# Optimization experiments

Hardware: AMD Instinct MI355X
Metric: run time of the kernel (lower is better)

The kernel has to match this reference:

```python
import jax, jax.numpy as jnp
import numpy as np

HIDDEN = 512
NHEADS = 8
ALPHA = 0.1
NUM_HOP = 4
MASK_VAL = -16384.0
LN_EPS = 1e-5


def setup_inputs() -> dict:
    key = jax.random.key(0)
    ks = jax.random.split(key, 10)
    B, N, H = 8, 1024, HIDDEN
    s = 1.0 / np.sqrt(H)
    x = jax.random.normal(ks[0], (B, N, H), dtype=jnp.float32)
    adj = jax.random.randint(ks[1], (B, N, N), 0, 2, dtype=jnp.int32)
    Wq = jax.random.uniform(ks[2], (H, H), jnp.float32, -s, s)
    bq = jax.random.uniform(ks[3], (H,), jnp.float32, -s, s)
    Wk = jax.random.uniform(ks[4], (H, H), jnp.float32, -s, s)
    bk = jax.random.uniform(ks[5], (H,), jnp.float32, -s, s)
    Wv = jax.random.uniform(ks[6], (H, H), jnp.float32, -s, s)
    bv = jax.random.uniform(ks[7], (H,), jnp.float32, -s, s)
    gamma = jnp.ones((H,), jnp.float32)
    beta = jnp.zeros((H,), jnp.float32)
    return {"x": x, "adj": adj, "Wq": Wq, "bq": bq, "Wk": Wk, "bk": bk,
            "Wv": Wv, "bv": bv, "gamma": gamma, "beta": beta}


def reference(x, adj, Wq, bq, Wk, bk, Wv, bv, gamma, beta):
    B, N, H = x.shape
    u = H // NHEADS
    # torch Linear: y = x @ W^T + b
    q = x @ Wq.T + bq  # [B,N,H]
    k = x @ Wk.T + bk
    v = x @ Wv.T + bv
    # split hidden into contiguous head chunks (matches per-head slicing)
    qh = q.reshape(B, N, NHEADS, u).transpose(0, 2, 1, 3)  # [B,Hd,N,u]
    kh = k.reshape(B, N, NHEADS, u).transpose(0, 2, 1, 3)
    vh = v.reshape(B, N, NHEADS, u).transpose(0, 2, 1, 3)
    scores = jnp.einsum('bhnd,bhmd->bhnm', qh, kh)  # [B,Hd,N,N]
    mask = (adj == 0)[:, None, :, :]  # broadcast over heads
    scores = jnp.where(mask, MASK_VAL, scores)
    pros = jax.nn.softmax(scores, axis=-1)
    z_init = vh
    z = z_init
    for _ in range(NUM_HOP):
        z = (1.0 - ALPHA) * jnp.einsum('bhnm,bhmd->bhnd', pros, z) + ALPHA * z_init
    h_prime = z.transpose(0, 2, 1, 3).reshape(B, N, H)  # concat heads
    y = x + h_prime
    mu = jnp.mean(y, axis=-1, keepdims=True)
    var = jnp.mean((y - mu) ** 2, axis=-1, keepdims=True)
    return (y - mu) / jnp.sqrt(var + LN_EPS) * gamma + beta
```

## Files before the change

kernel.cpp:

```cpp
#include <hip/hip_runtime.h>
#include <hip/hip_bf16.h>

#define BB 8
#define NN 1024
#define HH 512
#define NHEADS 8
#define UU 64

typedef __attribute__((ext_vector_type(8))) short short8;
typedef __attribute__((ext_vector_type(4))) float f32x4;
typedef unsigned short u16;
typedef unsigned char u8;

__device__ inline float b2f(unsigned short u) {
    union { float f; unsigned int i; } c; c.i = ((unsigned int)u) << 16; return c.f;
}
__device__ inline unsigned short f2b(float f) {
    __hip_bfloat16 h = __float2bfloat16(f);
    return *reinterpret_cast<unsigned short*>(&h);
}
__device__ inline void gl_lds16(const void* g, void* l) {
    __builtin_amdgcn_global_load_lds(
        (const __attribute__((address_space(1))) unsigned int*)g,
        (__attribute__((address_space(3))) unsigned int*)l, 16, 0, 0);
}

__global__ __launch_bounds__(256) void cvt_w(
    const float* __restrict__ Wq, const float* __restrict__ Wk,
    const float* __restrict__ Wv, u16* __restrict__ Wb)
{
    const int which = blockIdx.y;
    const float* src = which == 0 ? Wq : (which == 1 ? Wk : Wv);
    u16* dst = Wb + (size_t)which * HH * HH;
    const int base = (blockIdx.x * 256 + threadIdx.x) * 8;
    const float4* sp = (const float4*)&src[base];
    float4 a = sp[0], b = sp[1];
    short8 o;
    o[0] = (short)f2b(a.x); o[1] = (short)f2b(a.y);
    o[2] = (short)f2b(a.z); o[3] = (short)f2b(a.w);
    o[4] = (short)f2b(b.x); o[5] = (short)f2b(b.y);
    o[6] = (short)f2b(b.z); o[7] = (short)f2b(b.w);
    *(short8*)&dst[base] = o;
}

__global__ __launch_bounds__(256) void adj_pack(
    const int* __restrict__ adj, unsigned int* __restrict__ adjp)
{
    const int wave = threadIdx.x >> 6, lane = threadIdx.x & 63;
    const int row = blockIdx.x * 4 + wave;
    const int* ar = adj + (size_t)row * NN;
    unsigned long long* out = (unsigned long long*)(adjp + (size_t)row * 32);
    #pragma unroll
    for (int it = 0; it < 16; ++it) {
        int a = ar[it * 64 + lane];
        unsigned long long m = __ballot(a != 0);
        if (lane == 0) out[it] = m;
    }
}

__global__ __launch_bounds__(256) void qkv_gemm(
    const float* __restrict__ x, const u16* __restrict__ Wb,
    const float* __restrict__ bq, const float* __restrict__ bk,
    const float* __restrict__ bv,
    u16* __restrict__ q, u16* __restrict__ k, u16* __restrict__ v)
{
    const int which = blockIdx.z;
    const u16* W      = Wb + (size_t)which * HH * HH;
    const float* bias = which == 0 ? bq : (which == 1 ? bk : bv);
    u16* out          = which == 0 ? q  : (which == 1 ? k  : v);

    const int tid = threadIdx.x;
    const int wave = tid >> 6, lane = tid & 63;
    const int ln = lane & 15, quad = lane >> 4;
    const int wr = (wave >> 1) * 64, wc = (wave & 1) * 64;
    const int rowbase = blockIdx.x * 128, colbase = blockIdx.y * 128;

    __shared__ __align__(16) u16 As[128 * 40];
    __shared__ __align__(16) u16 Bs[128 * 32];
    __shared__ __align__(16) u16 Cs[128 * 136];

    f32x4 acc[4][4];
    #pragma unroll
    for (int ri = 0; ri < 4; ++ri)
        #pragma unroll
        for (int ci = 0; ci < 4; ++ci) acc[ri][ci] = (f32x4){0.f, 0.f, 0.f, 0.f};

    const int lr = lane >> 2;
    const int sg = lane & 3;

    for (int kk = 0; kk < HH; kk += 32) {
        __syncthreads();
        #pragma unroll
        for (int i = 0; i < 2; ++i) {
            int r = wave * 32 + i * 16 + lr;
            const float* xp = &x[(size_t)(rowbase + r) * HH + kk + sg * 8];
            float4 f0 = *(const float4*)xp, f1 = *(const float4*)(xp + 4);
            short8 o;
            o[0] = (short)f2b(f0.x); o[1] = (short)f2b(f0.y);
            o[2] = (short)f2b(f0.z); o[3] = (short)f2b(f0.w);
            o[4] = (short)f2b(f1.x); o[5] = (short)f2b(f1.y);
            o[6] = (short)f2b(f1.z); o[7] = (short)f2b(f1.w);
            *(short8*)&As[r * 40 + sg * 8] = o;
            gl_lds16(&W[(size_t)(colbase + r) * HH + kk + sg * 8],
                     (char*)Bs + (wave * 32 + i * 16) * 64);
        }
        __syncthreads();

        short8 bfr[4];
        #pragma unroll
        for (int ci = 0; ci < 4; ++ci)
            bfr[ci] = *(const short8*)&Bs[(wc + ci * 16 + ln) * 32 + quad * 8];
        #pragma unroll
        for (int ri = 0; ri < 4; ++ri) {
            short8 af = *(const short8*)&As[(wr + ri * 16 + ln) * 40 + quad * 8];
            #pragma unroll
            for (int ci = 0; ci < 4; ++ci)
                acc[ri][ci] = __builtin_amdgcn_mfma_f32_16x16x32_bf16(af, bfr[ci], acc[ri][ci], 0, 0, 0);
        }
    }

    #pragma unroll
    for (int ci = 0; ci < 4; ++ci) {
        int col = wc + ci * 16 + ln;
        float bb = bias[colbase + col];
        #pragma unroll
        for (int ri = 0; ri < 4; ++ri) {
            #pragma unroll
            for (int r = 0; r < 4; ++r) {
                int row = wr + ri * 16 + quad * 4 + r;
                Cs[row * 136 + col] = f2b(acc[ri][ci][r] + bb);
            }
        }
    }
    __syncthreads();
    {
        int row = tid >> 1, half = tid & 1;
        int gcol0 = colbase + half * 64;
        int hh = gcol0 >> 6;
        int grow = rowbase + row;
        int bidx = grow >> 10, n = grow & 1023;
        u16* op = &out[(((size_t)(bidx * NHEADS + hh)) * NN + n) * UU];
        const u16* cp = &Cs[row * 136 + half * 64];
        #pragma unroll
        for (int j = 0; j < 8; ++j)
            *(short8*)(op + j * 8) = *(const short8*)(cp + j * 8);
    }
}

__global__ __launch_bounds__(256) void vt8(
    const u16* __restrict__ v, u8* __restrict__ v8t)
{
    const int bh = blockIdx.x >> 2, part = blockIdx.x & 3;
    const int t = threadIdx.x;
    const size_t hd = (size_t)bh << 16;
    __shared__ u16 tile[64][72];

    for (int chunk = part * 4; chunk < part * 4 + 4; ++chunk) {
        const int n0 = chunk * 64;
        const int r = t >> 2, cs = t & 3;
        const u16* vp = &v[((size_t)bh * NN + n0 + r) * UU + cs * 16];
        short8 a = *(const short8*)vp;
        short8 b8 = *(const short8*)(vp + 8);
        #pragma unroll
        for (int j = 0; j < 8; ++j) {
            tile[r][cs * 16 + j] = (u16)a[j];
            tile[r][cs * 16 + 8 + j] = (u16)b8[j];
        }
        __syncthreads();
        const int c = t & 63, qt = t >> 6;
        unsigned int w[4];
        #pragma unroll
        for (int g = 0; g < 4; ++g) {
            float f0 = b2f(tile[qt * 16 + g * 4 + 0][c]);
            float f1 = b2f(tile[qt * 16 + g * 4 + 1][c]);
            float f2 = b2f(tile[qt * 16 + g * 4 + 2][c]);
            float f3 = b2f(tile[qt * 16 + g * 4 + 3][c]);
            int lo = __builtin_amdgcn_cvt_pk_fp8_f32(f0, f1, 0, false);
            w[g] = (unsigned int)__builtin_amdgcn_cvt_pk_fp8_f32(f2, f3, lo, true);
        }
        uint4 o; o.x = w[0]; o.y = w[1]; o.z = w[2]; o.w = w[3];
        *(uint4*)&v8t[hd + (size_t)c * 1024 + n0 + qt * 16] = o;
        __syncthreads();
    }
}

__global__ __launch_bounds__(256) void scores_softmax(
    const u16* __restrict__ q, const u16* __restrict__ kmat,
    const unsigned int* __restrict__ adjp, u8* __restrict__ P8)
{
    const int b = blockIdx.z, h = blockIdx.y, rt = blockIdx.x;
    const int bh = b * NHEADS + h;
    const int tid = threadIdx.x;
    const int wave = tid >> 6, lane = tid & 63;
    const int ln = lane & 15, quad = lane >> 4;
    const int wrow = rt * 64 + wave * 16;

    __shared__ __align__(16) u16 ks[128 * 72];
    __shared__ __align__(16) u16 eb[64 * 136];

    const u16* qp = &q[((size_t)bh * NN + wrow + ln) * UU + quad * 8];
    short8 a0 = *(const short8*)qp;
    short8 a1 = *(const short8*)(qp + 32);

    float rsum[4] = {0.f, 0.f, 0.f, 0.f};
    float scl[4];

    const int srow = tid >> 3;
    const int sseg = tid & 7;

    for (int pass = 0; pass < 2; ++pass) {
        for (int cc = 0; cc < 8; ++cc) {
            __syncthreads();
            #pragma unroll
            for (int j = 0; j < 4; ++j) {
                int kr = j * 32 + srow;
                uint4 kv = *(const uint4*)&kmat[((size_t)bh * NN + cc * 128 + kr) * UU + sseg * 8];
                *(uint4*)&ks[kr * 72 + sseg * 8] = kv;
            }
            __syncthreads();

            unsigned int ab[4][4];
            #pragma unroll
            for (int r = 0; r < 4; ++r) {
                int row = wrow + quad * 4 + r;
                *(uint4*)&ab[r][0] =
                    *(const uint4*)&adjp[((size_t)(b * NN + row)) * 32 + cc * 4];
            }

            #pragma unroll
            for (int ct = 0; ct < 8; ++ct) {
                const u16* kp = &ks[(ct * 16 + ln) * 72 + quad * 8];
                short8 b0 = *(const short8*)kp;
                short8 b1 = *(const short8*)(kp + 32);
                f32x4 acc = (f32x4){0.f, 0.f, 0.f, 0.f};
                acc = __builtin_amdgcn_mfma_f32_16x16x32_bf16(a0, b0, acc, 0, 0, 0);
                acc = __builtin_amdgcn_mfma_f32_16x16x32_bf16(a1, b1, acc, 0, 0, 0);
                const int dw = ct >> 1;
                const int bitpos = (ct & 1) * 16 + ln;
                #pragma unroll
                for (int r = 0; r < 4; ++r) {
                    unsigned int on = (ab[r][dw] >> bitpos) & 1u;
                    float e = on ? __expf(acc[r] - 32.0f) : 0.0f;
                    if (pass == 0) rsum[r] += e;
                    else eb[(wave * 16 + quad * 4 + r) * 136 + ct * 16 + ln] = f2b(e * scl[r]);
                }
            }

            if (pass == 1) {
                const int kcp = lane >> 4, r16 = lane & 15;
                const u16* ep = &eb[(wave * 16 + r16) * 136 + kcp * 32];
                unsigned int w[8];
                #pragma unroll
                for (int g2 = 0; g2 < 4; ++g2) {
                    short8 ev = *(const short8*)(ep + g2 * 8);
                    float f0 = b2f((u16)ev[0]);
                    float f1 = b2f((u16)ev[1]);
                    float f2 = b2f((u16)ev[2]);
                    float f3 = b2f((u16)ev[3]);
                    int lo = __builtin_amdgcn_cvt_pk_fp8_f32(f0, f1, 0, false);
                    w[g2 * 2] = (unsigned int)__builtin_amdgcn_cvt_pk_fp8_f32(f2, f3, lo, true);
                    f0 = b2f((u16)ev[4]);
                    f1 = b2f((u16)ev[5]);
                    f2 = b2f((u16)ev[6]);
                    f3 = b2f((u16)ev[7]);
                    lo = __builtin_amdgcn_cvt_pk_fp8_f32(f0, f1, 0, false);
                    w[g2 * 2 + 1] = (unsigned int)__builtin_amdgcn_cvt_pk_fp8_f32(f2, f3, lo, true);
                }
                u8* op = P8 + ((size_t)bh << 20) + (size_t)(rt * 4 + wave) * 16384
                       + (cc * 4 + kcp) * 512 + r16 * 32;
                uint4 o0; o0.x = w[0]; o0.y = w[1]; o0.z = w[2]; o0.w = w[3];
                uint4 o1; o1.x = w[4]; o1.y = w[5]; o1.z = w[6]; o1.w = w[7];
                *(uint4*)op = o0;
                *(uint4*)(op + 16) = o1;
            }
        }
        if (pass == 0) {
            #pragma unroll
            for (int r = 0; r < 4; ++r) {
                #pragma unroll
                for (int off = 8; off >= 1; off >>= 1)
                    rsum[r] += __shfl_xor(rsum[r], off);
                scl[r] = 16.0f / rsum[r];
            }
        }
    }
}

__global__ __launch_bounds__(512) void hop(
    const u8* __restrict__ P8, const u8* __restrict__ z8in,
    const u16* __restrict__ v, u8* __restrict__ z8out,
    u16* __restrict__ zbf_out, int last)
{
    const int b = blockIdx.z, h = blockIdx.y, rt = blockIdx.x;
    const int bh = b * NHEADS + h;
    const int tid = threadIdx.x;
    const int wave = tid >> 6, lane = tid & 63;
    const int ln = lane & 15, quad = lane >> 4;
    const int wrow = rt * 128 + wave * 16;

    __shared__ __align__(16) u8 zt[64 * 1040];

    const u8* zg = z8in + ((size_t)bh << 16);
    #pragma unroll
    for (int i = 0; i < 8; ++i) {
        int c = wave * 8 + i;
        gl_lds16(zg + (size_t)c * 1024 + lane * 16, (char*)zt + c * 1040);
    }
    __syncthreads();

    f32x4 acc[4];
    #pragma unroll
    for (int ci = 0; ci < 4; ++ci) acc[ci] = (f32x4){0.f, 0.f, 0.f, 0.f};

    const u8* pt = P8 + ((size_t)bh << 20) + (size_t)(rt * 8 + wave) * 16384
                 + ln * 32 + quad * 8;
    #pragma unroll 4
    for (int kc = 0; kc < 32; ++kc) {
        long a = *(const long*)(pt + kc * 512);
        int kk = kc * 32;
        #pragma unroll
        for (int ci = 0; ci < 4; ++ci) {
            long bz = *(const long*)&zt[(ci * 16 + ln) * 1040 + kk + quad * 8];
            acc[ci] = __builtin_amdgcn_mfma_f32_16x16x32_fp8_fp8(a, bz, acc[ci], 0, 0, 0);
        }
    }

    if (last) {
        #pragma unroll
        for (int ci = 0; ci < 4; ++ci) {
            int col = ci * 16 + ln;
            #pragma unroll
            for (int r = 0; r < 4; ++r) {
                int row = wrow + quad * 4 + r;
                float vv = b2f(v[((size_t)bh * NN + row) * UU + col]);
                zbf_out[((size_t)(b * NN + row)) * HH + h * UU + col]
                    = f2b(0.05625f * acc[ci][r] + 0.1f * vv);
            }
        }
    } else {
        u8* zo = z8out + ((size_t)bh << 16);
        #pragma unroll
        for (int ci = 0; ci < 4; ++ci) {
            int col = ci * 16 + ln;
            float zv[4];
            #pragma unroll
            for (int r = 0; r < 4; ++r) {
                int row = wrow + quad * 4 + r;
                float vv = b2f(v[((size_t)bh * NN + row) * UU + col]);
                zv[r] = 0.05625f * acc[ci][r] + 0.1f * vv;
            }
            int lo = __builtin_amdgcn_cvt_pk_fp8_f32(zv[0], zv[1], 0, false);
            unsigned int dw = (unsigned int)__builtin_amdgcn_cvt_pk_fp8_f32(zv[2], zv[3], lo, true);
            *(unsigned int*)&zo[(size_t)col * 1024 + wrow + quad * 4] = dw;
        }
    }
}

__global__ __launch_bounds__(256) void resid_ln(
    const float* __restrict__ x, const u16* __restrict__ z,
    const float* __restrict__ gamma, const float* __restrict__ beta,
    float* __restrict__ out)
{
    const int r = blockIdx.x * 4 + (threadIdx.x >> 6);
    const int lane = threadIdx.x & 63;
    const size_t base = (size_t)r * HH + lane * 8;

    const float4* xp = (const float4*)&x[base];
    float4 x0 = xp[0], x1 = xp[1];
    short8 zv = *(const short8*)&z[base];
    float y[8];
    y[0] = x0.x + b2f((u16)zv[0]); y[1] = x0.y + b2f((u16)zv[1]);
    y[2] = x0.z + b2f((u16)zv[2]); y[3] = x0.w + b2f((u16)zv[3]);
    y[4] = x1.x + b2f((u16)zv[4]); y[5] = x1.y + b2f((u16)zv[5]);
    y[6] = x1.z + b2f((u16)zv[6]); y[7] = x1.w + b2f((u16)zv[7]);

    float s = 0.f, sq = 0.f;
    #pragma unroll
    for (int j = 0; j < 8; ++j) { s += y[j]; sq += y[j] * y[j]; }
    #pragma unroll
    for (int off = 32; off >= 1; off >>= 1) {
        s  += __shfl_xor(s, off);
        sq += __shfl_xor(sq, off);
    }
    const float mu = s * (1.0f / HH);
    const float var = sq * (1.0f / HH) - mu * mu;
    const float rstd = rsqrtf(var + 1e-5f);

    const float4* gp = (const float4*)&gamma[lane * 8];
    const float4* bp = (const float4*)&beta[lane * 8];
    float4 g0 = gp[0], g1 = gp[1], b0 = bp[0], b1 = bp[1];

    float4 o0, o1;
    o0.x = (y[0] - mu) * rstd * g0.x + b0.x;
    o0.y = (y[1] - mu) * rstd * g0.y + b0.y;
    o0.z = (y[2] - mu) * rstd * g0.z + b0.z;
    o0.w = (y[3] - mu) * rstd * g0.w + b0.w;
    o1.x = (y[4] - mu) * rstd * g1.x + b1.x;
    o1.y = (y[5] - mu) * rstd * g1.y + b1.y;
    o1.z = (y[6] - mu) * rstd * g1.z + b1.z;
    o1.w = (y[7] - mu) * rstd * g1.w + b1.w;
    float4* op = (float4*)&out[base];
    op[0] = o0; op[1] = o1;
}

extern "C" void kernel_launch(void* const* d_in, const int* in_sizes, int n_in,
                              void* d_out, int out_size, void* d_ws, size_t ws_size,
                              hipStream_t stream)
{
    const float* x   = (const float*)d_in[0];
    const int* adj   = (const int*)d_in[1];
    const float* Wq  = (const float*)d_in[2];
    const float* bq  = (const float*)d_in[3];
    const float* Wk  = (const float*)d_in[4];
    const float* bk  = (const float*)d_in[5];
    const float* Wv  = (const float*)d_in[6];
    const float* bv  = (const float*)d_in[7];
    const float* gamma = (const float*)d_in[8];
    const float* beta  = (const float*)d_in[9];
    float* out = (float*)d_out;

    const size_t E = (size_t)BB * NN * HH;
    u16* ws16 = (u16*)d_ws;
    u16* q  = ws16 + E;
    u16* k  = ws16 + 2 * E;
    u16* v  = ws16 + 3 * E;
    u16* za = ws16 + 4 * E;
    u16* Wb = ws16 + 5 * E;
    u8* base8 = (u8*)(ws16 + 5 * E + 786432);
    u8* P8  = base8;
    u8* z8a = base8 + ((size_t)64 << 20);
    u8* z8b = z8a + ((size_t)4 << 20);
    u8* v8t = z8b + ((size_t)4 << 20);
    unsigned int* adjp = (unsigned int*)(v8t + ((size_t)4 << 20));

    cvt_w<<<dim3(128, 3), 256, 0, stream>>>(Wq, Wk, Wv, Wb);
    adj_pack<<<dim3(2048), 256, 0, stream>>>(adj, adjp);
    qkv_gemm<<<dim3(64, 4, 3), 256, 0, stream>>>(x, Wb, bq, bk, bv, q, k, v);
    vt8<<<dim3(256), 256, 0, stream>>>(v, v8t);
    scores_softmax<<<dim3(16, NHEADS, BB), 256, 0, stream>>>(q, k, adjp, P8);
    hop<<<dim3(8, NHEADS, BB), 512, 0, stream>>>(P8, v8t, v, z8a, za, 0);
    hop<<<dim3(8, NHEADS, BB), 512, 0, stream>>>(P8, z8a, v, z8b, za, 0);
    hop<<<dim3(8, NHEADS, BB), 512, 0, stream>>>(P8, z8b, v, z8a, za, 0);
    hop<<<dim3(8, NHEADS, BB), 512, 0, stream>>>(P8, z8a, v, z8b, za, 1);
    resid_ln<<<dim3(2048), 256, 0, stream>>>(x, za, gamma, beta, out);
}
```

Measured before the change: 287.9 us.

## Fuse four hop launches and LayerNorm into one persistent kernel with grid barriers

Merges the four hop kernels and the residual-LayerNorm kernel into one persistent kernel of 512 blocks. Each hop phase is separated by a software grid-wide barrier built from atomics in workspace, which is reset by a memset before the launch. The goal is to remove five kernel launch gaps and tail effects. It also overlaps the qkv_gemm As/Bs/Cs shared buffers into one array to cut LDS use, which needs an extra __syncthreads. The grid barrier relies on all 512 blocks being co-resident, so the kernel deadlocks if occupancy is lower than assumed.

```diff
diff --git a/kernel.cpp b/kernel.cpp
--- a/kernel.cpp
+++ b/kernel.cpp
@@ -75,9 +75,10 @@
     const int wr = (wave >> 1) * 64, wc = (wave & 1) * 64;
     const int rowbase = blockIdx.x * 128, colbase = blockIdx.y * 128;
 
-    __shared__ __align__(16) u16 As[128 * 40];
-    __shared__ __align__(16) u16 Bs[128 * 32];
-    __shared__ __align__(16) u16 Cs[128 * 136];
+    __shared__ __align__(16) u8 smem[128 * 136 * 2];
+    u16* As = (u16*)smem;
+    u16* Bs = (u16*)(smem + 10240);
+    u16* Cs = (u16*)smem;
 
     f32x4 acc[4][4];
     #pragma unroll
@@ -119,6 +120,7 @@
         }
     }
 
+    __syncthreads();
     #pragma unroll
     for (int ci = 0; ci < 4; ++ci) {
         int col = wc + ci * 16 + ln;
@@ -286,13 +288,35 @@
     }
 }
 
-__global__ __launch_bounds__(512) void hop(
-    const u8* __restrict__ P8, const u8* __restrict__ z8in,
-    const u16* __restrict__ v, u8* __restrict__ z8out,
-    u16* __restrict__ zbf_out, int last)
-{
-    const int b = blockIdx.z, h = blockIdx.y, rt = blockIdx.x;
-    const int bh = b * NHEADS + h;
+__device__ inline void gbar(unsigned int* bar, int phase, unsigned int nblk) {
+    __syncthreads();
+    if (threadIdx.x == 0) {
+        __threadfence();
+        unsigned int arr = __hip_atomic_fetch_add(&bar[phase * 2], 1u,
+                             __ATOMIC_ACQ_REL, __HIP_MEMORY_SCOPE_AGENT);
+        if (arr == nblk - 1) {
+            __hip_atomic_store(&bar[phase * 2 + 1], 1u,
+                               __ATOMIC_RELEASE, __HIP_MEMORY_SCOPE_AGENT);
+        } else {
+            while (__hip_atomic_load(&bar[phase * 2 + 1],
+                     __ATOMIC_ACQUIRE, __HIP_MEMORY_SCOPE_AGENT) == 0u)
+                __builtin_amdgcn_s_sleep(8);
+        }
+        __threadfence();
+    }
+    __syncthreads();
+}
+
+__global__ __launch_bounds__(512, 4) void hops_ln(
+    const u8* __restrict__ P8, const u8* __restrict__ v8t,
+    const u16* __restrict__ v, u8* __restrict__ z8a, u8* __restrict__ z8b,
+    u16* __restrict__ za, const float* __restrict__ x,
+    const float* __restrict__ gamma, const float* __restrict__ beta,
+    float* __restrict__ out, unsigned int* __restrict__ bar)
+{
+    const int blk = blockIdx.x;
+    const int bh = blk >> 3, rt = blk & 7;
+    const int b = bh >> 3, h = bh & 7;
     const int tid = threadIdx.x;
     const int wave = tid >> 6, lane = tid & 63;
     const int ln = lane & 15, quad = lane >> 4;
@@ -300,107 +324,107 @@
 
     __shared__ __align__(16) u8 zt[64 * 1040];
 
-    const u8* zg = z8in + ((size_t)bh << 16);
-    #pragma unroll
-    for (int i = 0; i < 8; ++i) {
-        int c = wave * 8 + i;
-        gl_lds16(zg + (size_t)c * 1024 + lane * 16, (char*)zt + c * 1040);
-    }
-    __syncthreads();
-
-    f32x4 acc[4];
-    #pragma unroll
-    for (int ci = 0; ci < 4; ++ci) acc[ci] = (f32x4){0.f, 0.f, 0.f, 0.f};
-
-    const u8* pt = P8 + ((size_t)bh << 20) + (size_t)(rt * 8 + wave) * 16384
-                 + ln * 32 + quad * 8;
-    #pragma unroll 4
-    for (int kc = 0; kc < 32; ++kc) {
-        long a = *(const long*)(pt + kc * 512);
-        int kk = kc * 32;
-        #pragma unroll
-        for (int ci = 0; ci < 4; ++ci) {
-            long bz = *(const long*)&zt[(ci * 16 + ln) * 1040 + kk + quad * 8];
-            acc[ci] = __builtin_amdgcn_mfma_f32_16x16x32_fp8_fp8(a, bz, acc[ci], 0, 0, 0);
-        }
-    }
-
-    if (last) {
-        #pragma unroll
-        for (int ci = 0; ci < 4; ++ci) {
-            int col = ci * 16 + ln;
-            #pragma unroll
-            for (int r = 0; r < 4; ++r) {
-                int row = wrow + quad * 4 + r;
-                float vv = b2f(v[((size_t)bh * NN + row) * UU + col]);
-                zbf_out[((size_t)(b * NN + row)) * HH + h * UU + col]
-                    = f2b(0.05625f * acc[ci][r] + 0.1f * vv);
-            }
-        }
-    } else {
-        u8* zo = z8out + ((size_t)bh << 16);
-        #pragma unroll
-        for (int ci = 0; ci < 4; ++ci) {
-            int col = ci * 16 + ln;
-            float zv[4];
-            #pragma unroll
-            for (int r = 0; r < 4; ++r) {
-                int row = wrow + quad * 4 + r;
-                float vv = b2f(v[((size_t)bh * NN + row) * UU + col]);
-                zv[r] = 0.05625f * acc[ci][r] + 0.1f * vv;
-            }
-            int lo = __builtin_amdgcn_cvt_pk_fp8_f32(zv[0], zv[1], 0, false);
-            unsigned int dw = (unsigned int)__builtin_amdgcn_cvt_pk_fp8_f32(zv[2], zv[3], lo, true);
-            *(unsigned int*)&zo[(size_t)col * 1024 + wrow + quad * 4] = dw;
-        }
-    }
-}
-
-__global__ __launch_bounds__(256) void resid_ln(
-    const float* __restrict__ x, const u16* __restrict__ z,
-    const float* __restrict__ gamma, const float* __restrict__ beta,
-    float* __restrict__ out)
-{
-    const int r = blockIdx.x * 4 + (threadIdx.x >> 6);
-    const int lane = threadIdx.x & 63;
-    const size_t base = (size_t)r * HH + lane * 8;
-
-    const float4* xp = (const float4*)&x[base];
-    float4 x0 = xp[0], x1 = xp[1];
-    short8 zv = *(const short8*)&z[base];
-    float y[8];
-    y[0] = x0.x + b2f((u16)zv[0]); y[1] = x0.y + b2f((u16)zv[1]);
-    y[2] = x0.z + b2f((u16)zv[2]); y[3] = x0.w + b2f((u16)zv[3]);
-    y[4] = x1.x + b2f((u16)zv[4]); y[5] = x1.y + b2f((u16)zv[5]);
-    y[6] = x1.z + b2f((u16)zv[6]); y[7] = x1.w + b2f((u16)zv[7]);
-
-    float s = 0.f, sq = 0.f;
-    #pragma unroll
-    for (int j = 0; j < 8; ++j) { s += y[j]; sq += y[j] * y[j]; }
-    #pragma unroll
-    for (int off = 32; off >= 1; off >>= 1) {
-        s  += __shfl_xor(s, off);
-        sq += __shfl_xor(sq, off);
-    }
-    const float mu = s * (1.0f / HH);
-    const float var = sq * (1.0f / HH) - mu * mu;
-    const float rstd = rsqrtf(var + 1e-5f);
-
-    const float4* gp = (const float4*)&gamma[lane * 8];
-    const float4* bp = (const float4*)&beta[lane * 8];
-    float4 g0 = gp[0], g1 = gp[1], b0 = bp[0], b1 = bp[1];
-
-    float4 o0, o1;
-    o0.x = (y[0] - mu) * rstd * g0.x + b0.x;
-    o0.y = (y[1] - mu) * rstd * g0.y + b0.y;
-    o0.z = (y[2] - mu) * rstd * g0.z + b0.z;
-    o0.w = (y[3] - mu) * rstd * g0.w + b0.w;
-    o1.x = (y[4] - mu) * rstd * g1.x + b1.x;
-    o1.y = (y[5] - mu) * rstd * g1.y + b1.y;
-    o1.z = (y[6] - mu) * rstd * g1.z + b1.z;
-    o1.w = (y[7] - mu) * rstd * g1.w + b1.w;
-    float4* op = (float4*)&out[base];
-    op[0] = o0; op[1] = o1;
+    const u8* zins[4]  = { v8t, z8a, z8b, z8a };
+    u8*       zouts[4] = { z8a, z8b, z8a, nullptr };
+
+    for (int ph = 0; ph < 4; ++ph) {
+        const u8* zg = zins[ph] + ((size_t)bh << 16);
+        #pragma unroll
+        for (int i = 0; i < 8; ++i) {
+            int c = wave * 8 + i;
+            gl_lds16(zg + (size_t)c * 1024 + lane * 16, (char*)zt + c * 1040);
+        }
+        __syncthreads();
+
+        f32x4 acc[4];
+        #pragma unroll
+        for (int ci = 0; ci < 4; ++ci) acc[ci] = (f32x4){0.f, 0.f, 0.f, 0.f};
+
+        const u8* pt = P8 + ((size_t)bh << 20) + (size_t)(rt * 8 + wave) * 16384
+                     + ln * 32 + quad * 8;
+        #pragma unroll 4
+        for (int kc = 0; kc < 32; ++kc) {
+            long a = *(const long*)(pt + kc * 512);
+            int kk = kc * 32;
+            #pragma unroll
+            for (int ci = 0; ci < 4; ++ci) {
+                long bz = *(const long*)&zt[(ci * 16 + ln) * 1040 + kk + quad * 8];
+                acc[ci] = __builtin_amdgcn_mfma_f32_16x16x32_fp8_fp8(a, bz, acc[ci], 0, 0, 0);
+            }
+        }
+
+        if (ph == 3) {
+            #pragma unroll
+            for (int ci = 0; ci < 4; ++ci) {
+                int col = ci * 16 + ln;
+                #pragma unroll
+                for (int r = 0; r < 4; ++r) {
+                    int row = wrow + quad * 4 + r;
+                    float vv = b2f(v[((size_t)bh * NN + row) * UU + col]);
+                    za[((size_t)(b * NN + row)) * HH + h * UU + col]
+                        = f2b(0.05625f * acc[ci][r] + 0.1f * vv);
+                }
+            }
+        } else {
+            u8* zo = zouts[ph] + ((size_t)bh << 16);
+            #pragma unroll
+            for (int ci = 0; ci < 4; ++ci) {
+                int col = ci * 16 + ln;
+                float zv[4];
+                #pragma unroll
+                for (int r = 0; r < 4; ++r) {
+                    int row = wrow + quad * 4 + r;
+                    float vv = b2f(v[((size_t)bh * NN + row) * UU + col]);
+                    zv[r] = 0.05625f * acc[ci][r] + 0.1f * vv;
+                }
+                int lo = __builtin_amdgcn_cvt_pk_fp8_f32(zv[0], zv[1], 0, false);
+                unsigned int dw = (unsigned int)__builtin_amdgcn_cvt_pk_fp8_f32(zv[2], zv[3], lo, true);
+                *(unsigned int*)&zo[(size_t)col * 1024 + wrow + quad * 4] = dw;
+            }
+        }
+        gbar(bar, ph, gridDim.x);
+    }
+
+    const int r0 = blk * 16;
+    for (int rr = wave; rr < 16; rr += 8) {
+        const int row = r0 + rr;
+        const size_t base = (size_t)row * HH + lane * 8;
+        const float4* xp = (const float4*)&x[base];
+        float4 x0 = xp[0], x1 = xp[1];
+        short8 zv = *(const short8*)&za[base];
+        float y[8];
+        y[0] = x0.x + b2f((u16)zv[0]); y[1] = x0.y + b2f((u16)zv[1]);
+        y[2] = x0.z + b2f((u16)zv[2]); y[3] = x0.w + b2f((u16)zv[3]);
+        y[4] = x1.x + b2f((u16)zv[4]); y[5] = x1.y + b2f((u16)zv[5]);
+        y[6] = x1.z + b2f((u16)zv[6]); y[7] = x1.w + b2f((u16)zv[7]);
+
+        float s = 0.f, sq = 0.f;
+        #pragma unroll
+        for (int j = 0; j < 8; ++j) { s += y[j]; sq += y[j] * y[j]; }
+        #pragma unroll
+        for (int off = 32; off >= 1; off >>= 1) {
+            s  += __shfl_xor(s, off);
+            sq += __shfl_xor(sq, off);
+        }
+        const float mu = s * (1.0f / HH);
+        const float var = sq * (1.0f / HH) - mu * mu;
+        const float rstd = rsqrtf(var + 1e-5f);
+
+        const float4* gp = (const float4*)&gamma[lane * 8];
+        const float4* bp = (const float4*)&beta[lane * 8];
+        float4 g0 = gp[0], g1 = gp[1], b0 = bp[0], b1 = bp[1];
+        float4 o0, o1;
+        o0.x = (y[0] - mu) * rstd * g0.x + b0.x;
+        o0.y = (y[1] - mu) * rstd * g0.y + b0.y;
+        o0.z = (y[2] - mu) * rstd * g0.z + b0.z;
+        o0.w = (y[3] - mu) * rstd * g0.w + b0.w;
+        o1.x = (y[4] - mu) * rstd * g1.x + b1.x;
+        o1.y = (y[5] - mu) * rstd * g1.y + b1.y;
+        o1.z = (y[6] - mu) * rstd * g1.z + b1.z;
+        o1.w = (y[7] - mu) * rstd * g1.w + b1.w;
+        float4* op = (float4*)&out[base];
+        op[0] = o0; op[1] = o1;
+    }
 }
 
 extern "C" void kernel_launch(void* const* d_in, const int* in_sizes, int n_in,
@@ -432,15 +456,14 @@
     u8* z8b = z8a + ((size_t)4 << 20);
     u8* v8t = z8b + ((size_t)4 << 20);
     unsigned int* adjp = (unsigned int*)(v8t + ((size_t)4 << 20));
-
+    unsigned int* bar  = (unsigned int*)((u8*)adjp + ((size_t)1 << 20));
+
+    hipMemsetAsync(bar, 0, 64, stream);
     cvt_w<<<dim3(128, 3), 256, 0, stream>>>(Wq, Wk, Wv, Wb);
     adj_pack<<<dim3(2048), 256, 0, stream>>>(adj, adjp);
     qkv_gemm<<<dim3(64, 4, 3), 256, 0, stream>>>(x, Wb, bq, bk, bv, q, k, v);
     vt8<<<dim3(256), 256, 0, stream>>>(v, v8t);
     scores_softmax<<<dim3(16, NHEADS, BB), 256, 0, stream>>>(q, k, adjp, P8);
-    hop<<<dim3(8, NHEADS, BB), 512, 0, stream>>>(P8, v8t, v, z8a, za, 0);
-    hop<<<dim3(8, NHEADS, BB), 512, 0, stream>>>(P8, z8a, v, z8b, za, 0);
-    hop<<<dim3(8, NHEADS, BB), 512, 0, stream>>>(P8, z8b, v, z8a, za, 0);
-    hop<<<dim3(8, NHEADS, BB), 512, 0, stream>>>(P8, z8a, v, z8b, za, 1);
-    resid_ln<<<dim3(2048), 256, 0, stream>>>(x, za, gamma, beta, out);
-}
+    hops_ln<<<dim3(512), 512, 0, stream>>>(P8, v8t, v, z8a, z8b, za,
+                                           x, gamma, beta, out, bar);
+}
```

After: 612.4 us. 2.13x slower.
